# Performance work log

Measured on AMD Instinct MI355X. Metric: run time of the kernel, lower is better.

## Reference

```python
import jax, jax.numpy as jnp
import numpy as np

B, D, L, K = 4096, 1024, 16384, 64


def setup_inputs() -> dict:
    key = jax.random.key(0)
    k1, k2, k3, k4, k5 = jax.random.split(key, 5)
    x = jax.random.normal(k1, (B, D), dtype=jnp.float32)
    # torch nn.Linear weights are [out_features, in_features]
    W_enc = jax.random.normal(k2, (L, D), dtype=jnp.float32) * (1.0 / np.sqrt(D))
    b_enc = jax.random.normal(k3, (L,), dtype=jnp.float32) * 0.01
    W_dec = jax.random.normal(k4, (D, L), dtype=jnp.float32) * (1.0 / np.sqrt(L))
    b_dec = jax.random.normal(k5, (D,), dtype=jnp.float32) * 0.01
    return {"x": x, "W_enc": W_enc, "b_enc": b_enc, "W_dec": W_dec, "b_dec": b_dec}


def reference(x, W_enc, b_enc, W_dec, b_dec):
    # xbar = x - decoder.bias
    xbar = x - b_dec                                   # [B, D]
    a = jnp.einsum('bd,ld->bl', xbar, W_enc) + b_enc   # [B, L]
    vals, idx = jax.lax.top_k(a, K)                    # [B, K]
    f = jnp.zeros_like(a)
    rows = jnp.arange(a.shape[0])[:, None]             # [B, 1]
    f = f.at[rows, idx].set(jax.nn.relu(vals))         # sparse latent [B, L]
    xhat = jnp.einsum('bl,dl->bd', f, W_dec) + b_dec   # [B, D]
    return (f, xhat)
```

## Files before the change

kernel.cpp:

```cpp
#include <hip/hip_runtime.h>

#define B_N 4096
#define D_N 1024
#define L_N 16384
#define K_N 64
#define CAP 512
#define CNT_STRIDE 16

typedef __attribute__((ext_vector_type(8))) short bf16x8;
typedef __attribute__((ext_vector_type(4))) float f32x4;

__device__ __forceinline__ unsigned short f2bf(float f) {
  union { float f; unsigned int u; } v; v.f = f;
  unsigned int r = v.u + 0x7FFFu + ((v.u >> 16) & 1u);
  return (unsigned short)(r >> 16);
}
__device__ __forceinline__ float bf2f(unsigned short u) {
  union { unsigned int u; float f; } v; v.u = (unsigned int)u << 16;
  return v.f;
}

__global__ __launch_bounds__(256) void prep_all(const float* __restrict__ x,
                                                const float* __restrict__ W_enc,
                                                const float* __restrict__ W_dec,
                                                const float* __restrict__ b_dec,
                                                unsigned short* __restrict__ wencb,
                                                unsigned short* __restrict__ xbarb,
                                                float* __restrict__ srow,
                                                unsigned short* __restrict__ WdTb,
                                                int* __restrict__ cand_cnt) {
  __shared__ float tile[32][33];
  __shared__ float wsum[4];
  const int t = threadIdx.x;
  const int bid = blockIdx.x;
  if (bid < 16384) {
    size_t i = (size_t)bid * 256 + t;
    float4 v = ((const float4*)W_enc)[i];
    ushort4 o;
    o.x = f2bf(v.x); o.y = f2bf(v.y); o.z = f2bf(v.z); o.w = f2bf(v.w);
    ((ushort4*)wencb)[i] = o;
  } else if (bid < 20480) {
    const int b = bid - 16384;
    if (t == 0) cand_cnt[b * CNT_STRIDE] = 0;
    float4 v = ((const float4*)x)[(size_t)b * 256 + t];
    float4 bd = ((const float4*)b_dec)[t];
    float4 e = make_float4(v.x - bd.x, v.y - bd.y, v.z - bd.z, v.w - bd.w);
    ushort4 o;
    o.x = f2bf(e.x); o.y = f2bf(e.y); o.z = f2bf(e.z); o.w = f2bf(e.w);
    ((ushort4*)xbarb)[(size_t)b * 256 + t] = o;
    float ss = e.x * e.x + e.y * e.y + e.z * e.z + e.w * e.w;
#pragma unroll
    for (int off = 32; off; off >>= 1) ss += __shfl_down(ss, off);
    if ((t & 63) == 0) wsum[t >> 6] = ss;
    __syncthreads();
    if (t == 0) srow[b] = sqrtf((wsum[0] + wsum[1] + wsum[2] + wsum[3]) * (1.0f / D_N));
  } else {
    const int tb = bid - 20480;
    const int l0 = (tb & 511) * 32;
    const int d0 = (tb >> 9) * 32;
    const int tx = t & 31, ty = t >> 5;
    for (int i = ty; i < 32; i += 8)
      tile[i][tx] = W_dec[(size_t)(d0 + i) * L_N + l0 + tx];
    __syncthreads();
    for (int i = ty; i < 32; i += 8)
      WdTb[(size_t)(l0 + i) * D_N + d0 + tx] = f2bf(tile[tx][i]);
  }
}

__global__ __launch_bounds__(512, 2) void gemm_enc_select(
    const unsigned short* __restrict__ A,
    const unsigned short* __restrict__ Bw,
    const float* __restrict__ b_enc,
    const float* __restrict__ srow,
    int* __restrict__ cand_cnt,
    float* __restrict__ cand_val,
    int* __restrict__ cand_idx) {
  __shared__ __align__(16) char smem[131072];
  const int tid = threadIdx.x;
  const int wid = tid >> 6, lane = tid & 63;
  const int wm = wid >> 2, wn = wid & 3;
  const int fr = lane & 15, quad = lane >> 4;

  const int wg = ((blockIdx.x & 7) << 7) + (blockIdx.x >> 3);
  const int bm = wg & 15, bn = wg >> 4;

  const int stgrow = wid * 8 + (lane >> 3);
  const int scol = ((lane & 7) ^ (lane >> 3)) << 4;
  const char* gA = (const char*)A + ((size_t)(bm * 256 + stgrow) * D_N) * 2 + scol;
  const char* gB = (const char*)Bw + ((size_t)(bn * 256 + stgrow) * D_N) * 2 + scol;

#define GLD(src_, dst_)                                                   \
  __builtin_amdgcn_global_load_lds(                                       \
      (const __attribute__((address_space(1))) void*)(src_),              \
      (__attribute__((address_space(3))) void*)(dst_), 16, 0, 0)

#define STGALL(po_, ko_)                                                              \
  {                                                                                   \
    _Pragma("unroll") for (int r_ = 0; r_ < 4; ++r_)                                  \
        GLD(gB + (size_t)r_ * 131072 + (ko_), smem + (po_) + 32768 + r_ * 8192 + wid * 1024); \
    _Pragma("unroll") for (int r_ = 0; r_ < 4; ++r_)                                  \
        GLD(gA + (size_t)r_ * 131072 + (ko_), smem + (po_) + r_ * 8192 + wid * 1024); \
  }

#define LDA(rh_, ks_)                                                                 \
  _Pragma("unroll") for (int i_ = 0; i_ < 4; ++i_)                                    \
      af[i_] = *(const bf16x8*)(smem + pb + (rh_)*16384 + aB + i_ * 2048 + (s0 ^ ((ks_)*64)));

#define LDB(dst_, ks_)                                                                \
  _Pragma("unroll") for (int j_ = 0; j_ < 4; ++j_)                                    \
      dst_[j_] = *(const bf16x8*)(smem + pb + bB + j_ * 2048 + (s0 ^ ((ks_)*64)));

#define MFMA16(rh_, bv_)                                                              \
  __builtin_amdgcn_s_setprio(1);                                                      \
  _Pragma("unroll") for (int i_ = 0; i_ < 4; ++i_)                                    \
      _Pragma("unroll") for (int j_ = 0; j_ < 4; ++j_)                                \
          acc[(rh_)*4 + i_][j_] = __builtin_amdgcn_mfma_f32_16x16x32_bf16(            \
              af[i_], bv_[j_], acc[(rh_)*4 + i_][j_], 0, 0, 0);                       \
  __builtin_amdgcn_s_setprio(0);

#define BAR __builtin_amdgcn_s_barrier()
#define LGKM0                                                                         \
  do {                                                                                \
    asm volatile("s_waitcnt lgkmcnt(0)" ::: "memory");                                \
    __builtin_amdgcn_sched_barrier(0);                                                \
  } while (0)
#define VMW(n_) asm volatile("s_waitcnt vmcnt(" #n_ ")" ::: "memory")

  f32x4 acc[8][4];
#pragma unroll
  for (int i = 0; i < 8; ++i)
#pragma unroll
    for (int j = 0; j < 4; ++j) acc[i][j] = (f32x4){0.f, 0.f, 0.f, 0.f};

  const int aB = (wm * 64 + fr) * 128;
  const int bB = 32768 + (wn * 64 + fr) * 128;
  const int s0 = (quad ^ (fr & 7)) << 4;

  STGALL(0, (size_t)0)
  VMW(2);
  BAR;

  for (int kt = 0; kt < 15; ++kt) {
    const int pb = (kt & 1) * 65536;
    const int po = pb ^ 65536;
    const size_t ko = (size_t)(kt + 1) * 128;
    bf16x8 af[4], bv0[4], bv1[4];
    LDA(0, 0) LDB(bv0, 0) STGALL(po, ko) BAR; LGKM0; MFMA16(0, bv0) BAR;
    LDA(0, 1) LDB(bv1, 1) BAR; LGKM0; MFMA16(0, bv1) VMW(8); BAR;
    LDA(1, 0) BAR; LGKM0; MFMA16(1, bv0) VMW(2); BAR;
    LDA(1, 1) BAR; LGKM0; MFMA16(1, bv1) BAR;
  }
  {
    const int pb = 65536;
    bf16x8 af[4], bv0[4], bv1[4];
    LDA(0, 0) LDB(bv0, 0) BAR; LGKM0; MFMA16(0, bv0) BAR;
    LDA(0, 1) LDB(bv1, 1) BAR; LGKM0; MFMA16(0, bv1) VMW(0); BAR;
    LDA(1, 0) BAR; LGKM0; MFMA16(1, bv0) BAR;
    LDA(1, 1) BAR; LGKM0; MFMA16(1, bv1)
  }

  const int lc0 = bn * 256 + wn * 64 + fr;
  float be[4];
#pragma unroll
  for (int nj = 0; nj < 4; ++nj) be[nj] = b_enc[lc0 + nj * 16];
#pragma unroll
  for (int mi = 0; mi < 8; ++mi) {
#pragma unroll
    for (int r = 0; r < 4; ++r) {
      const int grow = bm * 256 + (mi >> 2) * 128 + wm * 64 + (mi & 3) * 16 + quad * 4 + r;
      const float thr = 2.3f * srow[grow];
#pragma unroll
      for (int nj = 0; nj < 4; ++nj) {
        const float val = acc[mi][nj][r] + be[nj];
        if (val > thr) {
          const int p = atomicAdd(&cand_cnt[grow * CNT_STRIDE], 1);
          if (p < CAP) {
            cand_val[(size_t)grow * CAP + p] = val;
            cand_idx[(size_t)grow * CAP + p] = lc0 + nj * 16;
          }
        }
      }
    }
  }
#undef GLD
#undef STGALL
#undef LDA
#undef LDB
#undef MFMA16
#undef BAR
#undef LGKM0
#undef VMW
}

__global__ __launch_bounds__(256) void select_decode(
    const float* __restrict__ x,
    const float* __restrict__ W_enc,
    const float* __restrict__ b_enc,
    const float* __restrict__ b_dec,
    const float* __restrict__ srow,
    const int* __restrict__ cand_cnt,
    const float* __restrict__ cand_val,
    const int* __restrict__ cand_idx,
    const unsigned short* __restrict__ WdTb,
    float* __restrict__ f,
    float* __restrict__ xhat) {
  const int b = blockIdx.x, t = threadIdx.x;
  const int lane = t & 63, wave = t >> 6;
  __shared__ double xd[D_N];
  __shared__ float cv[CAP];
  __shared__ int ci[CAP];
  __shared__ double bu[128];
  __shared__ int bidx[128];
  __shared__ int o_idx[K_N];
  __shared__ float o_val[K_N];
  __shared__ int sidx[K_N];
  __shared__ float sval[K_N];
  __shared__ int nb_s, nin_s, outcnt;
  __shared__ float v64_s;

  {
    const float4 z4 = make_float4(0.f, 0.f, 0.f, 0.f);
    float4* frow = (float4*)(f + (size_t)b * L_N);
#pragma unroll
    for (int i = 0; i < 16; ++i) frow[i * 256 + t] = z4;
  }

  const int cnt = min(cand_cnt[b * CNT_STRIDE], CAP);
  if (t == 0) { nb_s = 0; nin_s = 0; outcnt = 0; v64_s = -1e30f; }
  for (int c = t; c < cnt; c += 256) {
    cv[c] = cand_val[(size_t)b * CAP + c];
    ci[c] = cand_idx[(size_t)b * CAP + c];
  }
  for (int i = t; i < D_N; i += 256)
    xd[i] = (double)x[(size_t)b * D_N + i] - (double)b_dec[i];
  __syncthreads();

  for (int c = t; c < cnt; c += 256) {
    const float v = cv[c];
    const int id = ci[c];
    int r = 0;
    for (int k = 0; k < cnt; ++k)
      r += (cv[k] > v || (cv[k] == v && ci[k] < id)) ? 1 : 0;
    if (r == 63) v64_s = v;
  }
  __syncthreads();
  const float v64 = v64_s;
  const float m = 0.04f * srow[b];

  for (int c = t; c < cnt; c += 256) {
    const float v = cv[c];
    if (v > v64 + m) {
      atomicAdd(&nin_s, 1);
    } else if (v >= v64 - m) {
      const int p = atomicAdd(&nb_s, 1);
      if (p < 128) bidx[p] = c;
    }
  }
  __syncthreads();
  const int nb = min(nb_s, 128);
  const int nin = nin_s;
  int nneed = K_N - nin;
  if (nneed < 0) nneed = 0;

  for (int c = wave; c < nb; c += 4) {
    const int l = ci[bidx[c]];
    const float4* wr = (const float4*)(W_enc + (size_t)l * D_N);
    double acc = 0.0;
#pragma unroll
    for (int j = 0; j < 4; ++j) {
      float4 w4 = wr[j * 64 + lane];
      const int base = (j * 64 + lane) * 4;
      acc += xd[base + 0] * (double)w4.x + xd[base + 1] * (double)w4.y +
             xd[base + 2] * (double)w4.z + xd[base + 3] * (double)w4.w;
    }
#pragma unroll
    for (int off = 32; off; off >>= 1) acc += __shfl_down(acc, off);
    if (lane == 0) bu[c] = acc + (double)b_enc[l];
  }
  __syncthreads();

  for (int c = t; c < cnt; c += 256) {
    if (cv[c] > v64 + m) {
      const int p = atomicAdd(&outcnt, 1);
      if (p < K_N) { o_idx[p] = ci[c]; o_val[p] = cv[c]; }
    }
  }
  if (t < nb) {
    const double uv = bu[t];
    const int l = ci[bidx[t]];
    int r = 0;
    for (int k = 0; k < nb; ++k)
      r += (bu[k] > uv || (bu[k] == uv && ci[bidx[k]] < l)) ? 1 : 0;
    if (r < nneed) {
      const int p = atomicAdd(&outcnt, 1);
      if (p < K_N) { o_idx[p] = l; o_val[p] = (float)uv; }
    }
  }
  __syncthreads();
  const int ns = min(outcnt, K_N);

  if (t < K_N) {
    sidx[t] = (t < ns) ? o_idx[t] : t;
    sval[t] = (t < ns) ? fmaxf(o_val[t], 0.0f) : 0.0f;
  }
  asm volatile("s_waitcnt vmcnt(0)" ::: "memory");
  __syncthreads();

  if (t < ns) f[(size_t)b * L_N + sidx[t]] = sval[t];

  float4 acc = ((const float4*)b_dec)[t];
#pragma unroll 8
  for (int k = 0; k < K_N; ++k) {
    const float v = sval[k];
    const ushort4 w = ((const ushort4*)(WdTb + (size_t)sidx[k] * D_N))[t];
    acc.x += v * bf2f(w.x); acc.y += v * bf2f(w.y);
    acc.z += v * bf2f(w.z); acc.w += v * bf2f(w.w);
  }
  ((float4*)(xhat + (size_t)b * D_N))[t] = acc;
}

extern "C" void kernel_launch(void* const* d_in, const int* in_sizes, int n_in,
                              void* d_out, int out_size, void* d_ws, size_t ws_size,
                              hipStream_t stream) {
  (void)in_sizes; (void)n_in; (void)out_size; (void)ws_size;
  const float* x     = (const float*)d_in[0];
  const float* W_enc = (const float*)d_in[1];
  const float* b_enc = (const float*)d_in[2];
  const float* W_dec = (const float*)d_in[3];
  const float* b_dec = (const float*)d_in[4];

  float* f    = (float*)d_out;
  float* xhat = (float*)d_out + (size_t)B_N * L_N;

  char* ws = (char*)d_ws;
  unsigned short* wencb = (unsigned short*)ws;
  unsigned short* xbarb = (unsigned short*)(ws + 33554432);
  unsigned short* WdTb  = (unsigned short*)(ws + 41943040);
  float* srow           = (float*)(ws + 75497472);
  int* cand_cnt         = (int*)(ws + 75513856);
  float* cand_val       = (float*)(ws + 75776000);
  int* cand_idx         = (int*)(ws + 84164608);

  prep_all<<<36864, 256, 0, stream>>>(x, W_enc, W_dec, b_dec, wencb, xbarb, srow,
                                      WdTb, cand_cnt);
  gemm_enc_select<<<1024, 512, 0, stream>>>(
      xbarb, wencb, b_enc, srow, cand_cnt, cand_val, cand_idx);
  select_decode<<<B_N, 256, 0, stream>>>(x, W_enc, b_enc, b_dec, srow,
                                         cand_cnt, cand_val, cand_idx, WdTb, f, xhat);
}
```

Measured before the change: 796.4 us.

## Split prep kernel, widen W_dec transpose tiles, use nontemporal output stores

Result: no change. 782.9 us (-1.7%).

```diff
diff --git a/kernel.cpp b/kernel.cpp
--- a/kernel.cpp
+++ b/kernel.cpp
@@ -19,51 +19,73 @@
   union { unsigned int u; float f; } v; v.u = (unsigned int)u << 16;
   return v.f;
 }
-
-__global__ __launch_bounds__(256) void prep_all(const float* __restrict__ x,
-                                                const float* __restrict__ W_enc,
-                                                const float* __restrict__ W_dec,
-                                                const float* __restrict__ b_dec,
-                                                unsigned short* __restrict__ wencb,
-                                                unsigned short* __restrict__ xbarb,
-                                                float* __restrict__ srow,
-                                                unsigned short* __restrict__ WdTb,
-                                                int* __restrict__ cand_cnt) {
-  __shared__ float tile[32][33];
-  __shared__ float wsum[4];
-  const int t = threadIdx.x;
-  const int bid = blockIdx.x;
-  if (bid < 16384) {
-    size_t i = (size_t)bid * 256 + t;
+__device__ __forceinline__ void nt_store4(float* p, float a, float b2, float c, float d) {
+  f32x4 v = {a, b2, c, d};
+  __builtin_nontemporal_store(v, (f32x4*)p);
+}
+
+__global__ __launch_bounds__(256) void prep_wenc(const float* __restrict__ W_enc,
+                                                 unsigned short* __restrict__ wencb) {
+  const size_t n4 = (size_t)L_N * D_N / 4;
+  for (size_t i = (size_t)blockIdx.x * 256 + threadIdx.x; i < n4; i += (size_t)2048 * 256) {
     float4 v = ((const float4*)W_enc)[i];
     ushort4 o;
     o.x = f2bf(v.x); o.y = f2bf(v.y); o.z = f2bf(v.z); o.w = f2bf(v.w);
     ((ushort4*)wencb)[i] = o;
-  } else if (bid < 20480) {
-    const int b = bid - 16384;
-    if (t == 0) cand_cnt[b * CNT_STRIDE] = 0;
-    float4 v = ((const float4*)x)[(size_t)b * 256 + t];
-    float4 bd = ((const float4*)b_dec)[t];
-    float4 e = make_float4(v.x - bd.x, v.y - bd.y, v.z - bd.z, v.w - bd.w);
-    ushort4 o;
-    o.x = f2bf(e.x); o.y = f2bf(e.y); o.z = f2bf(e.z); o.w = f2bf(e.w);
-    ((ushort4*)xbarb)[(size_t)b * 256 + t] = o;
-    float ss = e.x * e.x + e.y * e.y + e.z * e.z + e.w * e.w;
-#pragma unroll
-    for (int off = 32; off; off >>= 1) ss += __shfl_down(ss, off);
-    if ((t & 63) == 0) wsum[t >> 6] = ss;
-    __syncthreads();
-    if (t == 0) srow[b] = sqrtf((wsum[0] + wsum[1] + wsum[2] + wsum[3]) * (1.0f / D_N));
-  } else {
-    const int tb = bid - 20480;
-    const int l0 = (tb & 511) * 32;
-    const int d0 = (tb >> 9) * 32;
-    const int tx = t & 31, ty = t >> 5;
-    for (int i = ty; i < 32; i += 8)
-      tile[i][tx] = W_dec[(size_t)(d0 + i) * L_N + l0 + tx];
-    __syncthreads();
-    for (int i = ty; i < 32; i += 8)
-      WdTb[(size_t)(l0 + i) * D_N + d0 + tx] = f2bf(tile[tx][i]);
+  }
+}
+
+__global__ __launch_bounds__(256) void prep_xbar(const float* __restrict__ x,
+                                                 const float* __restrict__ b_dec,
+                                                 unsigned short* __restrict__ xbarb,
+                                                 float* __restrict__ srow,
+                                                 int* __restrict__ cand_cnt) {
+  __shared__ float wsum[4];
+  const int b = blockIdx.x, t = threadIdx.x;
+  if (t == 0) cand_cnt[b * CNT_STRIDE] = 0;
+  float4 v = ((const float4*)x)[(size_t)b * 256 + t];
+  float4 bd = ((const float4*)b_dec)[t];
+  float4 e = make_float4(v.x - bd.x, v.y - bd.y, v.z - bd.z, v.w - bd.w);
+  ushort4 o;
+  o.x = f2bf(e.x); o.y = f2bf(e.y); o.z = f2bf(e.z); o.w = f2bf(e.w);
+  ((ushort4*)xbarb)[(size_t)b * 256 + t] = o;
+  float ss = e.x * e.x + e.y * e.y + e.z * e.z + e.w * e.w;
+#pragma unroll
+  for (int off = 32; off; off >>= 1) ss += __shfl_down(ss, off);
+  if ((t & 63) == 0) wsum[t >> 6] = ss;
+  __syncthreads();
+  if (t == 0) srow[b] = sqrtf((wsum[0] + wsum[1] + wsum[2] + wsum[3]) * (1.0f / D_N));
+}
+
+__global__ __launch_bounds__(256) void prep_wdt(const float* __restrict__ W_dec,
+                                                unsigned short* __restrict__ WdTb) {
+  __shared__ float tile[64][65];
+  const int t = threadIdx.x;
+  const int l0 = (blockIdx.x >> 4) << 6;
+  const int d0 = (blockIdx.x & 15) << 6;
+  {
+    const int c4 = (t & 15) * 4;
+    const int r0 = t >> 4;
+#pragma unroll
+    for (int p = 0; p < 4; ++p) {
+      const int r = r0 + p * 16;
+      float4 v = *(const float4*)&W_dec[(size_t)(d0 + r) * L_N + l0 + c4];
+      tile[r][c4 + 0] = v.x; tile[r][c4 + 1] = v.y;
+      tile[r][c4 + 2] = v.z; tile[r][c4 + 3] = v.w;
+    }
+  }
+  __syncthreads();
+  {
+    const int j4 = (t & 15) * 4;
+    const int i0 = t >> 4;
+#pragma unroll
+    for (int p = 0; p < 4; ++p) {
+      const int i = i0 + p * 16;
+      ushort4 o;
+      o.x = f2bf(tile[j4 + 0][i]); o.y = f2bf(tile[j4 + 1][i]);
+      o.z = f2bf(tile[j4 + 2][i]); o.w = f2bf(tile[j4 + 3][i]);
+      *(ushort4*)&WdTb[(size_t)(l0 + i) * D_N + d0 + j4] = o;
+    }
   }
 }
 
@@ -219,10 +241,10 @@
   __shared__ float v64_s;
 
   {
-    const float4 z4 = make_float4(0.f, 0.f, 0.f, 0.f);
-    float4* frow = (float4*)(f + (size_t)b * L_N);
-#pragma unroll
-    for (int i = 0; i < 16; ++i) frow[i * 256 + t] = z4;
+    float* frow = f + (size_t)b * L_N;
+#pragma unroll
+    for (int i = 0; i < 16; ++i)
+      nt_store4(frow + (i * 256 + t) * 4, 0.f, 0.f, 0.f, 0.f);
   }
 
   const int cnt = min(cand_cnt[b * CNT_STRIDE], CAP);
@@ -316,7 +338,7 @@
     acc.x += v * bf2f(w.x); acc.y += v * bf2f(w.y);
     acc.z += v * bf2f(w.z); acc.w += v * bf2f(w.w);
   }
-  ((float4*)(xhat + (size_t)b * D_N))[t] = acc;
+  nt_store4(xhat + (size_t)b * D_N + t * 4, acc.x, acc.y, acc.z, acc.w);
 }
 
 extern "C" void kernel_launch(void* const* d_in, const int* in_sizes, int n_in,
@@ -341,10 +363,11 @@
   float* cand_val       = (float*)(ws + 75776000);
   int* cand_idx         = (int*)(ws + 84164608);
 
-  prep_all<<<36864, 256, 0, stream>>>(x, W_enc, W_dec, b_dec, wencb, xbarb, srow,
-                                      WdTb, cand_cnt);
+  prep_wenc<<<2048, 256, 0, stream>>>(W_enc, wencb);
+  prep_xbar<<<4096, 256, 0, stream>>>(x, b_dec, xbarb, srow, cand_cnt);
   gemm_enc_select<<<1024, 512, 0, stream>>>(
       xbarb, wencb, b_enc, srow, cand_cnt, cand_val, cand_idx);
+  prep_wdt<<<4096, 256, 0, stream>>>(W_dec, WdTb);
   select_decode<<<B_N, 256, 0, stream>>>(x, W_enc, b_enc, b_dec, srow,
                                          cand_cnt, cand_val, cand_idx, WdTb, f, xhat);
 }
```
